# Optimization experiments

Hardware: AMD Instinct MI355X
Metric: run time of the kernel (lower is better)

## Reference

```python
import jax, jax.numpy as jnp
import numpy as np

N_USER = 100000
N_ITEM = 50000
N = N_USER + N_ITEM
EMB = 64
FEAT = 384
NNZ = 2400000
N_PROMPT = 8
N_LAYERS = 4
EPS = 1e-8


def setup_inputs() -> dict:
    key = jax.random.key(0)
    ks = jax.random.split(key, 8)
    user_fea = jax.random.normal(ks[0], (N_USER, EMB), jnp.float32)
    item_fea = jax.random.normal(ks[1], (N_ITEM, FEAT), jnp.float32)
    prompt_embedding = jax.random.normal(ks[2], (N_PROMPT, EMB), jnp.float32)
    mlp_w = jax.random.normal(ks[3], (FEAT, EMB), jnp.float32) / np.sqrt(FEAT)
    mlp_b = jnp.zeros((EMB,), jnp.float32)
    adj_rows = jax.random.randint(ks[4], (NNZ,), 0, N, jnp.int32)
    adj_cols = jax.random.randint(ks[5], (NNZ,), 0, N, jnp.int32)
    # normalized-adjacency-like positive values
    adj_vals = jax.random.uniform(ks[6], (NNZ,), jnp.float32) * 0.01
    return dict(user_fea=user_fea, item_fea=item_fea,
                prompt_embedding=prompt_embedding, mlp_w=mlp_w, mlp_b=mlp_b,
                adj_rows=adj_rows, adj_cols=adj_cols, adj_vals=adj_vals)


def _spmm(rows, cols, vals, x):
    # sparse [N,N] @ dense [N,E] via gather + segment-sum
    return jax.ops.segment_sum(vals[:, None] * x[cols], rows, num_segments=N)


def reference(user_fea, item_fea, prompt_embedding, mlp_w, mlp_b,
              adj_rows, adj_cols, adj_vals):
    prompt_embd = jnp.sum(prompt_embedding, axis=0)            # [EMB]
    user_embd = user_fea + prompt_embd[None, :]                # [N_USER, EMB]
    item_embd = jnp.tanh(item_fea @ mlp_w + mlp_b)             # [N_ITEM, EMB]
    ego = jnp.concatenate([user_embd, item_embd], axis=0)      # [N, EMB]
    ego_norm = jnp.linalg.norm(ego, axis=-1)                   # [N]

    x = ego
    acc = ego  # running sum over layer stack (layer 0 = ego)
    for _ in range(N_LAYERS):
        x = _spmm(adj_rows, adj_cols, adj_vals, x)
        # cosine similarity of propagated embedding vs ego embedding, per row
        denom = jnp.maximum(jnp.linalg.norm(x, axis=-1) * ego_norm, EPS)
        w = jnp.sum(x * ego, axis=-1) / denom                  # [N]
        x = w[:, None] * x
        acc = acc + x

    return acc[:N_USER], acc[N_USER:]
```

## Files before the change

kernel.cpp:

```cpp
#include <hip/hip_runtime.h>
#include <hip/hip_fp16.h>

constexpr int kNUser = 100000;
constexpr int kNItem = 50000;
constexpr int kN     = 150000;
constexpr int kEmb   = 64;
constexpr int kFeat  = 384;
constexpr int kNnz   = 2400000;
constexpr float kEps = 1e-8f;

constexpr int kNBkt   = 256;
constexpr int kBR     = (kN + kNBkt - 1) / kNBkt;
constexpr int kChunkA = 4096;
constexpr int kNWGA   = (kNnz + kChunkA - 1) / kChunkA;

constexpr int kKS     = kFeat / 32;
constexpr int kNT     = kEmb / 16;
constexpr int kWElems = kKS * kNT * 64 * 8;

typedef __attribute__((ext_vector_type(8))) short short8v;
typedef __attribute__((ext_vector_type(4))) float floatx4;

__device__ inline unsigned short f2bf(float f) {
    unsigned u = __float_as_uint(f);
    return (unsigned short)((u + 0x7FFFu + ((u >> 16) & 1u)) >> 16);
}
__device__ inline float bf2f(unsigned short h) {
    return __uint_as_float((unsigned)h << 16);
}


__global__ void prompt_sum_k(const float* __restrict__ p, float* __restrict__ out) {
    int d = threadIdx.x;
    float s = 0.f;
#pragma unroll
    for (int i = 0; i < 8; ++i) s += p[i * kEmb + d];
    out[d] = s;
}

__global__ void user_ego_k(const float* __restrict__ uf, const float* __restrict__ ps,
                           float* __restrict__ ego) {
    int i = blockIdx.x * blockDim.x + threadIdx.x;
    if (i >= kNUser * kEmb) return;
    ego[i] = uf[i] + ps[i & 63];
}

__global__ void user_egoh_k(const float* __restrict__ uf, const float* __restrict__ ps,
                            unsigned short* __restrict__ egoh, float* __restrict__ nrm) {
    int wid  = threadIdx.x >> 6;
    int lane = threadIdx.x & 63;
    int row  = blockIdx.x * 4 + wid;
    if (row >= kNUser) return;
    size_t idx = (size_t)row * kEmb + lane;
    float e = uf[idx] + ps[lane];
    __half h = __float2half_rn(e);
    egoh[idx] = *(unsigned short*)&h;
    float s = e * e;
#pragma unroll
    for (int o = 32; o >= 1; o >>= 1) s += __shfl_xor(s, o, 64);
    if (lane == 0) nrm[row] = sqrtf(s);
}

__global__ void wsplit_k(const float* __restrict__ w, unsigned short* __restrict__ whi,
                         unsigned short* __restrict__ wlo) {
    int t = blockIdx.x * 256 + threadIdx.x;
    if (t >= kWElems) return;
    int j    = t & 7;
    int lane = (t >> 3) & 63;
    int nt   = (t >> 9) & 3;
    int ks   = t >> 11;
    int k = ks * 32 + (lane >> 4) * 8 + j;
    int n = nt * 16 + (lane & 15);
    float v = w[k * kEmb + n];
    unsigned short h = f2bf(v);
    whi[t] = h;
    wlo[t] = f2bf(v - bf2f(h));
}

__global__ __launch_bounds__(256)
void item_ego_mfma_k(const float* __restrict__ itf, const unsigned short* __restrict__ whi,
                     const unsigned short* __restrict__ wlo, const float* __restrict__ b,
                     unsigned short* __restrict__ egoh, float* __restrict__ nrm) {
    int t    = threadIdx.x;
    int wid  = t >> 6;
    int lane = t & 63;
    int r0   = blockIdx.x * 64 + wid * 16;
    int arow = r0 + (lane & 15);
    int kg   = lane >> 4;
    bool av  = arow < kNItem;
    const float* ap = itf + (size_t)(av ? arow : 0) * kFeat + kg * 8;

    const short8v* whv = (const short8v*)whi;
    const short8v* wlv = (const short8v*)wlo;

    floatx4 accH[kNT], accL[kNT];
#pragma unroll
    for (int nt = 0; nt < kNT; ++nt) {
        accH[nt] = (floatx4){0.f, 0.f, 0.f, 0.f};
        accL[nt] = (floatx4){0.f, 0.f, 0.f, 0.f};
    }

    for (int ks = 0; ks < kKS; ++ks) {
        const float4 z = make_float4(0.f, 0.f, 0.f, 0.f);
        float4 a0 = av ? *(const float4*)(ap + ks * 32)     : z;
        float4 a1 = av ? *(const float4*)(ap + ks * 32 + 4) : z;
        short8v ah, al;
#pragma unroll
        for (int j = 0; j < 8; ++j) {
            float f = (j < 4) ? ((const float*)&a0)[j] : ((const float*)&a1)[j - 4];
            unsigned short h = f2bf(f);
            ah[j] = (short)h;
            al[j] = (short)f2bf(f - bf2f(h));
        }
#pragma unroll
        for (int nt = 0; nt < kNT; ++nt) {
            short8v bh = whv[(ks * kNT + nt) * 64 + lane];
            short8v bl = wlv[(ks * kNT + nt) * 64 + lane];
            accH[nt] = __builtin_amdgcn_mfma_f32_16x16x32_bf16(ah, bh, accH[nt], 0, 0, 0);
            accL[nt] = __builtin_amdgcn_mfma_f32_16x16x32_bf16(ah, bl, accL[nt], 0, 0, 0);
            accL[nt] = __builtin_amdgcn_mfma_f32_16x16x32_bf16(al, bh, accL[nt], 0, 0, 0);
        }
    }

    int col0 = lane & 15;
    int rsub = (lane >> 4) * 4;
    float sq[4] = {0.f, 0.f, 0.f, 0.f};
#pragma unroll
    for (int nt = 0; nt < kNT; ++nt) {
        float bb = b[nt * 16 + col0];
#pragma unroll
        for (int r = 0; r < 4; ++r) {
            int row = r0 + rsub + r;
            float v = tanhf(accH[nt][r] + accL[nt][r] + bb);
            sq[r] = fmaf(v, v, sq[r]);
            if (row < kNItem) {
                __half h = __float2half_rn(v);
                egoh[(size_t)(kNUser + row) * kEmb + nt * 16 + col0] =
                    *(unsigned short*)&h;
            }
        }
    }
#pragma unroll
    for (int r = 0; r < 4; ++r) {
#pragma unroll
        for (int o = 1; o <= 8; o <<= 1) sq[r] += __shfl_xor(sq[r], o, 64);
        int row = r0 + rsub + r;
        if (col0 == 0 && row < kNItem) nrm[kNUser + row] = sqrtf(sq[r]);
    }
}

constexpr int kRW      = 16;
constexpr int kRowsBlk = 64;
constexpr int kKc      = 32;

__global__ __launch_bounds__(256, 2)
void item_ego_k(const float* __restrict__ itf, const float* __restrict__ w,
                const float* __restrict__ b, float* __restrict__ ego) {
    __shared__ float lds_a[kRowsBlk * kKc];
    int t      = threadIdx.x;
    int wid    = t >> 6;
    int lane   = t & 63;
    int blk_r0 = blockIdx.x * kRowsBlk;

    float acc[kRW];
#pragma unroll
    for (int r = 0; r < kRW; ++r) acc[r] = 0.f;

    int srow = t >> 3;
    int scol = (t & 7) * 4;

    for (int kc = 0; kc < kFeat; kc += kKc) {
        __syncthreads();
        {
            const float4 z = make_float4(0.f, 0.f, 0.f, 0.f);
            int gr0 = blk_r0 + srow;
            int gr1 = gr0 + 32;
            float4 v0 = (gr0 < kNItem)
                ? *(const float4*)(itf + (size_t)gr0 * kFeat + kc + scol) : z;
            float4 v1 = (gr1 < kNItem)
                ? *(const float4*)(itf + (size_t)gr1 * kFeat + kc + scol) : z;
            *(float4*)(lds_a + srow * kKc + scol)        = v0;
            *(float4*)(lds_a + (srow + 32) * kKc + scol) = v1;
        }
        float wreg[kKc];
#pragma unroll
        for (int k = 0; k < kKc; ++k) wreg[k] = w[(kc + k) * kEmb + lane];
        __syncthreads();
#pragma unroll
        for (int r = 0; r < kRW; ++r) {
            const float4* av = (const float4*)(lds_a + (wid * kRW + r) * kKc);
#pragma unroll
            for (int q = 0; q < 8; ++q) {
                float4 a = av[q];
                acc[r] = fmaf(a.x, wreg[q * 4 + 0], acc[r]);
                acc[r] = fmaf(a.y, wreg[q * 4 + 1], acc[r]);
                acc[r] = fmaf(a.z, wreg[q * 4 + 2], acc[r]);
                acc[r] = fmaf(a.w, wreg[q * 4 + 3], acc[r]);
            }
        }
    }
    float bv = b[lane];
#pragma unroll
    for (int r = 0; r < kRW; ++r) {
        int row = blk_r0 + wid * kRW + r;
        if (row < kNItem)
            ego[(size_t)(kNUser + row) * kEmb + lane] = tanhf(acc[r] + bv);
    }
}


__global__ __launch_bounds__(256)
void bcnt_k(const int* __restrict__ rows, int* __restrict__ bcnt) {
    __shared__ int cnt[kNBkt];
    int t  = threadIdx.x;
    int e0 = blockIdx.x * kChunkA;
    for (int i = t; i < kNBkt; i += 256) cnt[i] = 0;
    __syncthreads();
#pragma unroll
    for (int k = 0; k < kChunkA / 256; ++k) {
        int e = e0 + k * 256 + t;
        if (e < kNnz) atomicAdd(&cnt[rows[e] / kBR], 1);
    }
    __syncthreads();
    for (int i = t; i < kNBkt; i += 256)
        if (cnt[i]) atomicAdd(&bcnt[i], cnt[i]);
}

__global__ void bscan_k(const int* __restrict__ bcnt, int* __restrict__ bbase,
                        int* __restrict__ bfill) {
    __shared__ int sd[kNBkt];
    int t = threadIdx.x;
    int v = bcnt[t];
    sd[t] = v;
    __syncthreads();
#pragma unroll
    for (int off = 1; off < kNBkt; off <<= 1) {
        int u = (t >= off) ? sd[t - off] : 0;
        __syncthreads();
        sd[t] += u;
        __syncthreads();
    }
    bbase[t] = sd[t] - v;
    if (t == kNBkt - 1) bbase[kNBkt] = kNnz;
    bfill[t] = 0;
}

__global__ __launch_bounds__(256)
void bucket_k(const int* __restrict__ rows, const int* __restrict__ cols,
              const float* __restrict__ vals, const int* __restrict__ bbase,
              int* __restrict__ bfill, int2* __restrict__ tmp) {
    __shared__ int cnt[kNBkt];
    __shared__ int wgbase[kNBkt];
    int t  = threadIdx.x;
    int e0 = blockIdx.x * kChunkA;
    for (int i = t; i < kNBkt; i += 256) cnt[i] = 0;
    __syncthreads();
    int myb[kChunkA / 256];
    int myoff[kChunkA / 256];
#pragma unroll
    for (int k = 0; k < kChunkA / 256; ++k) {
        int e = e0 + k * 256 + t;
        if (e < kNnz) {
            int b = rows[e] / kBR;
            myb[k]   = b;
            myoff[k] = atomicAdd(&cnt[b], 1);
        } else {
            myb[k] = -1;
        }
    }
    __syncthreads();
    for (int i = t; i < kNBkt; i += 256)
        wgbase[i] = cnt[i] ? atomicAdd(&bfill[i], cnt[i]) : 0;
    __syncthreads();
#pragma unroll
    for (int k = 0; k < kChunkA / 256; ++k) {
        int b = myb[k];
        if (b < 0) continue;
        int e = e0 + k * 256 + t;
        int pos = bbase[b] + wgbase[b] + myoff[k];
        int rowrel = rows[e] - b * kBR;
        tmp[pos] = make_int2((rowrel << 18) | cols[e], __float_as_int(vals[e]));
    }
}

__global__ __launch_bounds__(256)
void debucket2_k(const int2* __restrict__ tmp, const int* __restrict__ bbase,
                 int* __restrict__ rp, int2* __restrict__ csr) {
    __shared__ int rcnt[kBR];
    __shared__ int rbaseL[kBR];
    __shared__ int sd[256];
    int b  = blockIdx.x;
    int t  = threadIdx.x;
    int j0 = bbase[b];
    int j1 = bbase[b + 1];
    for (int i = t; i < kBR; i += 256) rcnt[i] = 0;
    __syncthreads();
    for (int j = j0 + t; j < j1; j += 256)
        atomicAdd(&rcnt[(unsigned)tmp[j].x >> 18], 1);
    __syncthreads();
    int base = t * 3;
    int c0 = (base     < kBR) ? rcnt[base]     : 0;
    int c1 = (base + 1 < kBR) ? rcnt[base + 1] : 0;
    int c2 = (base + 2 < kBR) ? rcnt[base + 2] : 0;
    int tsum = c0 + c1 + c2;
    sd[t] = tsum;
    __syncthreads();
#pragma unroll
    for (int off = 1; off < 256; off <<= 1) {
        int u = (t >= off) ? sd[t - off] : 0;
        __syncthreads();
        sd[t] += u;
        __syncthreads();
    }
    int g0 = j0 + sd[t] - tsum;
    if (base     < kBR) rbaseL[base]     = g0;
    if (base + 1 < kBR) rbaseL[base + 1] = g0 + c0;
    if (base + 2 < kBR) rbaseL[base + 2] = g0 + c0 + c1;
    __syncthreads();
    int rbaseG = b * kBR;
    for (int i = t; i < kBR; i += 256) {
        int r = rbaseG + i;
        if (r < kN) rp[r] = rbaseL[i];
    }
    if (b == kNBkt - 1 && t == 0) rp[kN] = kNnz;
    for (int i = t; i < kBR; i += 256) rcnt[i] = 0;
    __syncthreads();
    for (int j = j0 + t; j < j1; j += 256) {
        int2 e = tmp[j];
        int rr = (unsigned)e.x >> 18;
        int pos = rbaseL[rr] + atomicAdd(&rcnt[rr], 1);
        csr[pos] = make_int2(e.x & 0x3FFFF, e.y);
    }
}

__global__ __launch_bounds__(256)
void layer_k(const int* __restrict__ rp, const int2* __restrict__ csr,
             const unsigned short* __restrict__ egoh, const float* __restrict__ nrm,
             const unsigned short* __restrict__ xin_h,
             unsigned short* __restrict__ xout_h,
             const unsigned short* __restrict__ xh1,
             const unsigned short* __restrict__ xh2,
             float* __restrict__ acc, int last) {
    int wid  = threadIdx.x >> 6;
    int lane = threadIdx.x & 63;
    int row  = blockIdx.x * 4 + wid;
    if (row >= kN) return;
    int q   = lane >> 4;
    int sub = lane & 15;
    int p0 = rp[row];
    int p1 = rp[row + 1];

    float4 s = make_float4(0.f, 0.f, 0.f, 0.f);
    for (int base = p0; base < p1; base += 16) {
        int2  e[4];
        float w[4];
#pragma unroll
        for (int g = 0; g < 4; ++g) {
            int j  = base + g * 4 + q;
            bool v = j < p1;
            e[g] = csr[v ? j : p0];
            w[g] = v ? __int_as_float(e[g].y) : 0.f;
        }
        uint2 gv[4];
#pragma unroll
        for (int g = 0; g < 4; ++g)
            gv[g] = *(const uint2*)(xin_h + (size_t)e[g].x * kEmb + sub * 4);
#pragma unroll
        for (int g = 0; g < 4; ++g) {
            float2 f0 = __half22float2(*(const __half2*)&gv[g].x);
            float2 f1 = __half22float2(*(const __half2*)&gv[g].y);
            s.x = fmaf(w[g], f0.x, s.x);
            s.y = fmaf(w[g], f0.y, s.y);
            s.z = fmaf(w[g], f1.x, s.z);
            s.w = fmaf(w[g], f1.y, s.w);
        }
    }
#pragma unroll
    for (int o = 16; o <= 32; o <<= 1) {
        s.x += __shfl_xor(s.x, o, 64);
        s.y += __shfl_xor(s.y, o, 64);
        s.z += __shfl_xor(s.z, o, 64);
        s.w += __shfl_xor(s.w, o, 64);
    }
    size_t idx = (size_t)row * kEmb + sub * 4;
    uint2 evu = *(const uint2*)(egoh + idx);
    float2 ea = __half22float2(*(const __half2*)&evu.x);
    float2 eb = __half22float2(*(const __half2*)&evu.y);
    float4 ev = make_float4(ea.x, ea.y, eb.x, eb.y);
    float d = s.x * ev.x + s.y * ev.y + s.z * ev.z + s.w * ev.w;
    float n = s.x * s.x + s.y * s.y + s.z * s.z + s.w * s.w;
#pragma unroll
    for (int o = 1; o <= 8; o <<= 1) {
        d += __shfl_xor(d, o, 64);
        n += __shfl_xor(n, o, 64);
    }
    float wgt = d / fmaxf(sqrtf(n) * nrm[row], kEps);
    if (q == 0) {
        float4 xw = make_float4(wgt * s.x, wgt * s.y, wgt * s.z, wgt * s.w);
        if (!last) {
            __half2 o0 = __floats2half2_rn(xw.x, xw.y);
            __half2 o1 = __floats2half2_rn(xw.z, xw.w);
            uint2 st;
            st.x = *(unsigned*)&o0;
            st.y = *(unsigned*)&o1;
            *(uint2*)(xout_h + idx) = st;
        } else {
            uint2 a1 = *(const uint2*)(xh1 + idx);
            uint2 a2 = *(const uint2*)(xh2 + idx);
            uint2 a3 = *(const uint2*)(xin_h + idx);
            float2 f1a = __half22float2(*(const __half2*)&a1.x);
            float2 f1b = __half22float2(*(const __half2*)&a1.y);
            float2 f2a = __half22float2(*(const __half2*)&a2.x);
            float2 f2b = __half22float2(*(const __half2*)&a2.y);
            float2 f3a = __half22float2(*(const __half2*)&a3.x);
            float2 f3b = __half22float2(*(const __half2*)&a3.y);
            float4 out;
            out.x = ev.x + f1a.x + f2a.x + f3a.x + xw.x;
            out.y = ev.y + f1a.y + f2a.y + f3a.y + xw.y;
            out.z = ev.z + f1b.x + f2b.x + f3b.x + xw.z;
            out.w = ev.w + f1b.y + f2b.y + f3b.y + xw.w;
            *(float4*)(acc + idx) = out;
        }
    }
}


__global__ void norm_init_full_k(const float* __restrict__ ego, float* __restrict__ nrm,
                                 float* __restrict__ x, float* __restrict__ acc) {
    int wid  = threadIdx.x >> 6;
    int lane = threadIdx.x & 63;
    int row  = blockIdx.x * 4 + wid;
    if (row >= kN) return;
    size_t idx = (size_t)row * kEmb + lane;
    float e = ego[idx];
    x[idx]   = e;
    acc[idx] = e;
    float s = e * e;
#pragma unroll
    for (int o = 32; o >= 1; o >>= 1) s += __shfl_xor(s, o, 64);
    if (lane == 0) nrm[row] = sqrtf(s);
}

__global__ void spmm_k(const int* __restrict__ rows, const int* __restrict__ cols,
                       const float* __restrict__ vals, const float* __restrict__ x,
                       float* __restrict__ y) {
    long long t = (long long)blockIdx.x * blockDim.x + threadIdx.x;
    int e = (int)(t >> 6);
    if (e >= kNnz) return;
    int lane = threadIdx.x & 63;
    atomicAdd(y + (size_t)rows[e] * kEmb + lane, vals[e] * x[(size_t)cols[e] * kEmb + lane]);
}

__global__ void weight_k(const float* __restrict__ ego, const float* __restrict__ nrm,
                         const float* __restrict__ y, float* __restrict__ x,
                         float* __restrict__ acc) {
    int wid  = threadIdx.x >> 6;
    int lane = threadIdx.x & 63;
    int row  = blockIdx.x * 4 + wid;
    if (row >= kN) return;
    size_t idx = (size_t)row * kEmb + lane;
    float yv = y[idx];
    float ev = ego[idx];
    float d = yv * ev;
    float n = yv * yv;
#pragma unroll
    for (int o = 32; o >= 1; o >>= 1) {
        d += __shfl_xor(d, o, 64);
        n += __shfl_xor(n, o, 64);
    }
    float w  = d / fmaxf(sqrtf(n) * nrm[row], kEps);
    float xw = w * yv;
    x[idx] = xw;
    acc[idx] += xw;
}


extern "C" void kernel_launch(void* const* d_in, const int* in_sizes, int n_in,
                              void* d_out, int out_size, void* d_ws, size_t ws_size,
                              hipStream_t stream) {
    const float* user_fea = (const float*)d_in[0];
    const float* item_fea = (const float*)d_in[1];
    const float* prompt   = (const float*)d_in[2];
    const float* mlp_w    = (const float*)d_in[3];
    const float* mlp_b    = (const float*)d_in[4];
    const int*   adj_rows = (const int*)d_in[5];
    const int*   adj_cols = (const int*)d_in[6];
    const float* adj_vals = (const float*)d_in[7];
    float* acc = (float*)d_out;

    const size_t NE = (size_t)kN * kEmb;
    float* ws = (float*)d_ws;

    size_t off = 0;
    float* f_ps  = ws + off; off += 64;
    float* f_nrm = ws + off; off += kN;
    size_t branch0 = off;
    unsigned short* f_egoh = (unsigned short*)(ws + off); off += NE / 2;
    unsigned short* f_xh1  = (unsigned short*)(ws + off); off += NE / 2;
    unsigned short* f_xh2  = (unsigned short*)(ws + off); off += NE / 2;
    unsigned short* f_xh3  = (unsigned short*)(ws + off); off += NE / 2;
    int* row_ptr = (int*)(ws + off); off += kN + 1;
    int* bcnt    = (int*)(ws + off); off += kNBkt;
    int* bbase   = (int*)(ws + off); off += kNBkt + 1;
    int* bfill   = (int*)(ws + off); off += kNBkt;
    off = (off + 3) & ~(size_t)3;
    unsigned short* whi = (unsigned short*)(ws + off); off += kWElems / 2;
    unsigned short* wlo = (unsigned short*)(ws + off); off += kWElems / 2;
    off = (off + 1) & ~(size_t)1;
    int2* csr = (int2*)(ws + off); off += (size_t)kNnz * 2;
    const bool use_csr = ws_size >= off * 4;

    prompt_sum_k<<<1, 64, 0, stream>>>(prompt, f_ps);

    if (use_csr) {
        user_egoh_k<<<(kNUser + 3) / 4, 256, 0, stream>>>(user_fea, f_ps,
                                                          f_egoh, f_nrm);
        wsplit_k<<<(kWElems + 255) / 256, 256, 0, stream>>>(mlp_w, whi, wlo);
        item_ego_mfma_k<<<(kNItem + 63) / 64, 256, 0, stream>>>(item_fea, whi, wlo,
                                                                mlp_b, f_egoh, f_nrm);

        int2* tmp = (int2*)f_xh1;
        hipMemsetAsync(bcnt, 0, kNBkt * sizeof(int), stream);
        bcnt_k<<<kNWGA, 256, 0, stream>>>(adj_rows, bcnt);
        bscan_k<<<1, kNBkt, 0, stream>>>(bcnt, bbase, bfill);
        bucket_k<<<kNWGA, 256, 0, stream>>>(adj_rows, adj_cols, adj_vals,
                                            bbase, bfill, tmp);
        debucket2_k<<<kNBkt, 256, 0, stream>>>(tmp, bbase, row_ptr, csr);

        layer_k<<<(kN + 3) / 4, 256, 0, stream>>>(row_ptr, csr, f_egoh, f_nrm,
                                                  f_egoh, f_xh1, nullptr, nullptr,
                                                  acc, 0);
        layer_k<<<(kN + 3) / 4, 256, 0, stream>>>(row_ptr, csr, f_egoh, f_nrm,
                                                  f_xh1, f_xh2, nullptr, nullptr,
                                                  acc, 0);
        layer_k<<<(kN + 3) / 4, 256, 0, stream>>>(row_ptr, csr, f_egoh, f_nrm,
                                                  f_xh2, f_xh3, nullptr, nullptr,
                                                  acc, 0);
        layer_k<<<(kN + 3) / 4, 256, 0, stream>>>(row_ptr, csr, f_egoh, f_nrm,
                                                  f_xh3, nullptr, f_xh1, f_xh2,
                                                  acc, 1);
    } else {
        float* f_ego = ws + branch0;
        float* f_x   = f_ego + NE;
        float* f_y   = f_x + NE;
        user_ego_k<<<(kNUser * kEmb + 255) / 256, 256, 0, stream>>>(user_fea, f_ps,
                                                                    f_ego);
        item_ego_k<<<(kNItem + kRowsBlk - 1) / kRowsBlk, 256, 0, stream>>>(
            item_fea, mlp_w, mlp_b, f_ego);
        norm_init_full_k<<<(kN + 3) / 4, 256, 0, stream>>>(f_ego, f_nrm, f_x, acc);
        for (int l = 0; l < 4; ++l) {
            hipMemsetAsync(f_y, 0, NE * sizeof(float), stream);
            spmm_k<<<(int)(((long long)kNnz * 64 + 255) / 256), 256, 0, stream>>>(
                adj_rows, adj_cols, adj_vals, f_x, f_y);
            weight_k<<<(kN + 3) / 4, 256, 0, stream>>>(f_ego, f_nrm, f_y, f_x, acc);
        }
    }
}
```

Measured before the change: 687.7 us.

## Map one CSR row per 16-lane quarter-wave in SpMM layer kernel

The layer kernel now gives each row to a 16-lane quarter of a wavefront, so each wave handles four rows instead of one. Each lane walks 16 edges per iteration with 16 gathers in flight, and the cross-quarter shuffle reduction is gone; all lanes now write their output slice. The aim is more memory parallelism per lane and less reduction overhead. The risks are higher register pressure and divergence when the four rows sharing a wave have different degrees.

```diff
diff --git a/kernel.cpp b/kernel.cpp
--- a/kernel.cpp
+++ b/kernel.cpp
@@ -343,44 +343,37 @@
              float* __restrict__ acc, int last) {
     int wid  = threadIdx.x >> 6;
     int lane = threadIdx.x & 63;
-    int row  = blockIdx.x * 4 + wid;
+    int qrow = lane >> 4;
+    int sub  = lane & 15;
+    int row  = blockIdx.x * 16 + wid * 4 + qrow;
     if (row >= kN) return;
-    int q   = lane >> 4;
-    int sub = lane & 15;
     int p0 = rp[row];
     int p1 = rp[row + 1];
 
     float4 s = make_float4(0.f, 0.f, 0.f, 0.f);
     for (int base = p0; base < p1; base += 16) {
-        int2  e[4];
-        float w[4];
-#pragma unroll
-        for (int g = 0; g < 4; ++g) {
-            int j  = base + g * 4 + q;
+        int2 e[16];
+#pragma unroll
+        for (int g = 0; g < 16; ++g) {
+            int j  = base + g;
             bool v = j < p1;
             e[g] = csr[v ? j : p0];
-            w[g] = v ? __int_as_float(e[g].y) : 0.f;
-        }
-        uint2 gv[4];
-#pragma unroll
-        for (int g = 0; g < 4; ++g)
+            if (!v) e[g].y = 0;
+        }
+        uint2 gv[16];
+#pragma unroll
+        for (int g = 0; g < 16; ++g)
             gv[g] = *(const uint2*)(xin_h + (size_t)e[g].x * kEmb + sub * 4);
 #pragma unroll
-        for (int g = 0; g < 4; ++g) {
+        for (int g = 0; g < 16; ++g) {
+            float w = __int_as_float(e[g].y);
             float2 f0 = __half22float2(*(const __half2*)&gv[g].x);
             float2 f1 = __half22float2(*(const __half2*)&gv[g].y);
-            s.x = fmaf(w[g], f0.x, s.x);
-            s.y = fmaf(w[g], f0.y, s.y);
-            s.z = fmaf(w[g], f1.x, s.z);
-            s.w = fmaf(w[g], f1.y, s.w);
-        }
-    }
-#pragma unroll
-    for (int o = 16; o <= 32; o <<= 1) {
-        s.x += __shfl_xor(s.x, o, 64);
-        s.y += __shfl_xor(s.y, o, 64);
-        s.z += __shfl_xor(s.z, o, 64);
-        s.w += __shfl_xor(s.w, o, 64);
+            s.x = fmaf(w, f0.x, s.x);
+            s.y = fmaf(w, f0.y, s.y);
+            s.z = fmaf(w, f1.x, s.z);
+            s.w = fmaf(w, f1.y, s.w);
+        }
     }
     size_t idx = (size_t)row * kEmb + sub * 4;
     uint2 evu = *(const uint2*)(egoh + idx);
@@ -395,32 +388,30 @@
         n += __shfl_xor(n, o, 64);
     }
     float wgt = d / fmaxf(sqrtf(n) * nrm[row], kEps);
-    if (q == 0) {
-        float4 xw = make_float4(wgt * s.x, wgt * s.y, wgt * s.z, wgt * s.w);
-        if (!last) {
-            __half2 o0 = __floats2half2_rn(xw.x, xw.y);
-            __half2 o1 = __floats2half2_rn(xw.z, xw.w);
-            uint2 st;
-            st.x = *(unsigned*)&o0;
-            st.y = *(unsigned*)&o1;
-            *(uint2*)(xout_h + idx) = st;
-        } else {
-            uint2 a1 = *(const uint2*)(xh1 + idx);
-            uint2 a2 = *(const uint2*)(xh2 + idx);
-            uint2 a3 = *(const uint2*)(xin_h + idx);
-            float2 f1a = __half22float2(*(const __half2*)&a1.x);
-            float2 f1b = __half22float2(*(const __half2*)&a1.y);
-            float2 f2a = __half22float2(*(const __half2*)&a2.x);
-            float2 f2b = __half22float2(*(const __half2*)&a2.y);
-            float2 f3a = __half22float2(*(const __half2*)&a3.x);
-            float2 f3b = __half22float2(*(const __half2*)&a3.y);
-            float4 out;
-            out.x = ev.x + f1a.x + f2a.x + f3a.x + xw.x;
-            out.y = ev.y + f1a.y + f2a.y + f3a.y + xw.y;
-            out.z = ev.z + f1b.x + f2b.x + f3b.x + xw.z;
-            out.w = ev.w + f1b.y + f2b.y + f3b.y + xw.w;
-            *(float4*)(acc + idx) = out;
-        }
+    float4 xw = make_float4(wgt * s.x, wgt * s.y, wgt * s.z, wgt * s.w);
+    if (!last) {
+        __half2 o0 = __floats2half2_rn(xw.x, xw.y);
+        __half2 o1 = __floats2half2_rn(xw.z, xw.w);
+        uint2 st;
+        st.x = *(unsigned*)&o0;
+        st.y = *(unsigned*)&o1;
+        *(uint2*)(xout_h + idx) = st;
+    } else {
+        uint2 a1 = *(const uint2*)(xh1 + idx);
+        uint2 a2 = *(const uint2*)(xh2 + idx);
+        uint2 a3 = *(const uint2*)(xin_h + idx);
+        float2 f1a = __half22float2(*(const __half2*)&a1.x);
+        float2 f1b = __half22float2(*(const __half2*)&a1.y);
+        float2 f2a = __half22float2(*(const __half2*)&a2.x);
+        float2 f2b = __half22float2(*(const __half2*)&a2.y);
+        float2 f3a = __half22float2(*(const __half2*)&a3.x);
+        float2 f3b = __half22float2(*(const __half2*)&a3.y);
+        float4 out;
+        out.x = ev.x + f1a.x + f2a.x + f3a.x + xw.x;
+        out.y = ev.y + f1a.y + f2a.y + f3a.y + xw.y;
+        out.z = ev.z + f1b.x + f2b.x + f3b.x + xw.z;
+        out.w = ev.w + f1b.y + f2b.y + f3b.y + xw.w;
+        *(float4*)(acc + idx) = out;
     }
 }
 
@@ -527,18 +518,19 @@
                                             bbase, bfill, tmp);
         debucket2_k<<<kNBkt, 256, 0, stream>>>(tmp, bbase, row_ptr, csr);
 
-        layer_k<<<(kN + 3) / 4, 256, 0, stream>>>(row_ptr, csr, f_egoh, f_nrm,
-                                                  f_egoh, f_xh1, nullptr, nullptr,
-                                                  acc, 0);
-        layer_k<<<(kN + 3) / 4, 256, 0, stream>>>(row_ptr, csr, f_egoh, f_nrm,
-                                                  f_xh1, f_xh2, nullptr, nullptr,
-                                                  acc, 0);
-        layer_k<<<(kN + 3) / 4, 256, 0, stream>>>(row_ptr, csr, f_egoh, f_nrm,
-                                                  f_xh2, f_xh3, nullptr, nullptr,
-                                                  acc, 0);
-        layer_k<<<(kN + 3) / 4, 256, 0, stream>>>(row_ptr, csr, f_egoh, f_nrm,
-                                                  f_xh3, nullptr, f_xh1, f_xh2,
-                                                  acc, 1);
+        const int grid = (kN + 15) / 16;
+        layer_k<<<grid, 256, 0, stream>>>(row_ptr, csr, f_egoh, f_nrm,
+                                          f_egoh, f_xh1, nullptr, nullptr,
+                                          acc, 0);
+        layer_k<<<grid, 256, 0, stream>>>(row_ptr, csr, f_egoh, f_nrm,
+                                          f_xh1, f_xh2, nullptr, nullptr,
+                                          acc, 0);
+        layer_k<<<grid, 256, 0, stream>>>(row_ptr, csr, f_egoh, f_nrm,
+                                          f_xh2, f_xh3, nullptr, nullptr,
+                                          acc, 0);
+        layer_k<<<grid, 256, 0, stream>>>(row_ptr, csr, f_egoh, f_nrm,
+                                          f_xh3, nullptr, f_xh1, f_xh2,
+                                          acc, 1);
     } else {
         float* f_ego = ws + branch0;
         float* f_x   = f_ego + NE;
```

New measurement: 691.9 us. Within noise of the previous version (+0.6%).
